# Kernel optimization log

Hardware: AMD Instinct MI355X
Metric: run time of the kernel (lower is better)

Reference implementation:

```python
import jax, jax.numpy as jnp
import numpy as np

B, T, D, H = 2, 4096, 512, 8
DH = D // H  # dim_head = 64


def setup_inputs() -> dict:
    key = jax.random.key(0)
    ks = jax.random.split(key, 10)
    s = 1.0 / np.sqrt(D)
    x = jax.random.normal(ks[0], (B, T, D), dtype=jnp.float32)
    Wq = jax.random.uniform(ks[1], (D, D), jnp.float32, -s, s)
    Wk = jax.random.uniform(ks[2], (D, D), jnp.float32, -s, s)
    Wv = jax.random.uniform(ks[3], (D, D), jnp.float32, -s, s)
    Wo = jax.random.uniform(ks[4], (D, D), jnp.float32, -s, s)
    bq = jnp.zeros((D,), jnp.float32)
    bk = jnp.zeros((D,), jnp.float32)
    bv = jnp.zeros((D,), jnp.float32)
    bo = jnp.zeros((D,), jnp.float32)
    mask = jax.random.randint(ks[5], (1, 1, T, T), 0, 2).astype(bool)
    return {"x": x, "Wq": Wq, "bq": bq, "Wk": Wk, "bk": bk,
            "Wv": Wv, "bv": bv, "Wo": Wo, "bo": bo, "mask": mask}


def reference(x, Wq, bq, Wk, bk, Wv, bv, Wo, bo, mask):
    # QKV projections (self-attention: Q=K=V=x)
    def split_heads(t):
        return t.reshape(B, T, H, DH).transpose(0, 2, 1, 3)  # (B,H,T,DH)
    Q = split_heads(x @ Wq + bq)
    K = split_heads(x @ Wk + bk)
    V = split_heads(x @ Wv + bv)
    # scaled dot-product attention with additive mask penalty (as in source)
    scores = jnp.einsum('bhqd,bhkd->bhqk', Q, K) / np.sqrt(DH)
    scores = scores + (~mask).astype(scores.dtype) * (-1e9)
    att_w = jax.nn.softmax(scores, axis=-1)
    O = jnp.einsum('bhqk,bhkd->bhqd', att_w, V)
    O = O.transpose(0, 2, 1, 3).reshape(B, T, D)
    return O @ Wo + bo
```

## Files before the change

### kernel.cpp

```cpp
#include <hip/hip_runtime.h>
#include <stdint.h>

#define B_ 2
#define T_ 4096
#define D_ 512
#define H_ 8
#define DH_ 64

typedef __bf16 bf16;
typedef __bf16 bf16x4_t __attribute__((ext_vector_type(4)));
typedef __bf16 bf16x8_t __attribute__((ext_vector_type(8)));
typedef float f32x4 __attribute__((ext_vector_type(4)));
typedef short short4_t __attribute__((ext_vector_type(4)));
typedef uint32_t u32;

static constexpr float QSCALE = 0.18033688011112042f;

__device__ __forceinline__ void async16(void* lds, const void* g) {
  __builtin_amdgcn_global_load_lds(
      (const __attribute__((address_space(1))) void*)g,
      (__attribute__((address_space(3))) void*)lds, 16, 0, 0);
}

__global__ __launch_bounds__(256) void prep_kernel(
    const float* __restrict__ x,
    const float* __restrict__ Wq, const float* __restrict__ Wk,
    const float* __restrict__ Wv, const float* __restrict__ Wo,
    const void* __restrict__ maskp,
    bf16* __restrict__ xb, bf16* __restrict__ WTall, bf16* __restrict__ WoT,
    u32* __restrict__ bmask)
{
  int bid = blockIdx.x;
  int tid = threadIdx.x;
  if (bid < 4096) {
    int idx = bid * 256 + tid;
    const float4* xf = (const float4*)x;
    float4 v = xf[idx];
    bf16x4_t o;
    o[0] = (bf16)v.x; o[1] = (bf16)v.y; o[2] = (bf16)v.z; o[3] = (bf16)v.w;
    ((bf16x4_t*)xb)[idx] = o;
  } else if (bid < 8192) {
    int gid = (bid - 4096) * 256 + tid;
    int sel = gid >> 18;
    int idx = gid & 262143;
    int n = idx >> 9, k = idx & 511;
    if (sel < 3) {
      const float* W = (sel == 0) ? Wq : (sel == 1) ? Wk : Wv;
      float v = W[k * 512 + n];
      if (sel == 0) v *= QSCALE;
      WTall[gid] = (bf16)v;
    } else {
      WoT[idx] = (bf16)Wo[k * 512 + n];
    }
  } else {
    int wid = (bid - 8192) * 256 + tid;
    const uint8_t* m8 = (const uint8_t*)maskp;
    bool u8mode = (__ballot(m8[4 * (tid & 63) + 1] != 0) != 0ull);
    int row = wid >> 7, wcol = wid & 127;
    size_t off = (size_t)row * 4096 + (size_t)wcol * 32;
    u32 w = 0;
    if (u8mode) {
      const uint4* p = (const uint4*)(m8 + off);
      uint4 a = p[0], b = p[1];
      u32 ws[8] = {a.x, a.y, a.z, a.w, b.x, b.y, b.z, b.w};
      #pragma unroll
      for (int j = 0; j < 32; ++j)
        if ((ws[j >> 2] >> ((j & 3) * 8)) & 0xffu) w |= (1u << j);
    } else {
      const uint4* p = (const uint4*)((const u32*)maskp + off);
      #pragma unroll
      for (int q = 0; q < 8; ++q) {
        uint4 a = p[q];
        if (a.x) w |= 1u << (q * 4 + 0);
        if (a.y) w |= 1u << (q * 4 + 1);
        if (a.z) w |= 1u << (q * 4 + 2);
        if (a.w) w |= 1u << (q * 4 + 3);
      }
    }
    bmask[((size_t)(row >> 6) * 64 + (wcol >> 1)) * 128 + (row & 63) * 2 + (wcol & 1)] = w;
  }
}

__global__ __launch_bounds__(256) void qkv_kernel(
    const bf16* __restrict__ xb, const bf16* __restrict__ WTall,
    const float* __restrict__ bq, const float* __restrict__ bk,
    const float* __restrict__ bv,
    bf16* __restrict__ Qb, bf16* __restrict__ Kb, bf16* __restrict__ Vtb)
{
  __shared__ char smem[32768];
  char* smX = smem;
  char* smW = smem + 16384;
  int tid = threadIdx.x;
  int lane = tid & 63, wave = tid >> 6;
  int lo = lane & 15, quad = lane >> 4;
  int wr = wave >> 1, wc = wave & 1;
  int bm = blockIdx.x * 128;
  int bn = blockIdx.y * 128;
  int sel = bn >> 9;
  f32x4 acc[4][4] = {};
  for (int kc = 0; kc < 8; ++kc) {
    __syncthreads();
    for (int s = tid; s < 1024; s += 256) {
      int row = s >> 3, slot = s & 7, cg = slot ^ (row & 7);
      async16(smX + s * 16, xb + (size_t)(bm + row) * 512 + kc * 64 + cg * 8);
      async16(smW + s * 16, WTall + (size_t)(bn + row) * 512 + kc * 64 + cg * 8);
    }
    __syncthreads();
    #pragma unroll
    for (int ks = 0; ks < 2; ++ks) {
      bf16x8_t a[4], b[4];
      #pragma unroll
      for (int mt = 0; mt < 4; ++mt) {
        int row = wr * 64 + mt * 16 + lo;
        int ch = (ks * 4 + quad) ^ (row & 7);
        a[mt] = *(const bf16x8_t*)(smX + row * 128 + ch * 16);
      }
      #pragma unroll
      for (int nt = 0; nt < 4; ++nt) {
        int row = wc * 64 + nt * 16 + lo;
        int ch = (ks * 4 + quad) ^ (row & 7);
        b[nt] = *(const bf16x8_t*)(smW + row * 128 + ch * 16);
      }
      if (sel == 2) {
        #pragma unroll
        for (int mt = 0; mt < 4; ++mt)
          #pragma unroll
          for (int nt = 0; nt < 4; ++nt)
            acc[mt][nt] = __builtin_amdgcn_mfma_f32_16x16x32_bf16(
                b[nt], a[mt], acc[mt][nt], 0, 0, 0);
      } else {
        #pragma unroll
        for (int mt = 0; mt < 4; ++mt)
          #pragma unroll
          for (int nt = 0; nt < 4; ++nt)
            acc[mt][nt] = __builtin_amdgcn_mfma_f32_16x16x32_bf16(
                a[mt], b[nt], acc[mt][nt], 0, 0, 0);
      }
    }
  }
  int b_ = bm >> 12;
  if (sel < 2) {
    #pragma unroll
    for (int mt = 0; mt < 4; ++mt) {
      #pragma unroll
      for (int nt = 0; nt < 4; ++nt) {
        int n0 = (bn + wc * 64 + nt * 16 + lo) & 511;
        int h = n0 >> 6, dh = n0 & 63;
        int m0 = bm + wr * 64 + mt * 16 + quad * 4;
        int t0 = m0 & 4095;
        float bias = (sel == 0) ? QSCALE * bq[n0] : bk[n0];
        bf16* dst = (sel == 0 ? Qb : Kb) + (size_t)(b_ * H_ + h) * T_ * DH_ + dh;
        #pragma unroll
        for (int r = 0; r < 4; ++r)
          dst[(size_t)(t0 + r) * 64] = (bf16)(acc[mt][nt][r] + bias);
      }
    }
  } else {
    #pragma unroll
    for (int mt = 0; mt < 4; ++mt) {
      #pragma unroll
      for (int nt = 0; nt < 4; ++nt) {
        int t0 = (bm & 4095) + wr * 64 + mt * 16 + lo;
        #pragma unroll
        for (int r = 0; r < 4; ++r) {
          int n0 = (bn & 511) + wc * 64 + nt * 16 + quad * 4 + r;
          float v = acc[mt][nt][r] + bv[n0];
          Vtb[((size_t)(b_ * H_ + (n0 >> 6)) * DH_ + (n0 & 63)) * T_ + t0] = (bf16)v;
        }
      }
    }
  }
}

__global__ __launch_bounds__(256, 4) void attn_kernel(
    const bf16* __restrict__ Qb, const bf16* __restrict__ Kb,
    const bf16* __restrict__ Vtb, const u32* __restrict__ bm2,
    bf16* __restrict__ Obuf)
{
  __shared__ char smem[16896];
  char* smK = smem;
  char* smV = smem + 8192;
  u32* smM = (u32*)(smem + 16384);
  int tid = threadIdx.x;
  int lane = tid & 63, wave = tid >> 6;
  int lo = lane & 15, quad = lane >> 4;
  int qh = wave & 1, kh = wave >> 1;
  int bh = blockIdx.x >> 6;
  int qt64 = blockIdx.x & 63;
  int qbase = qt64 * 64;

  const bf16* Qg = Qb + ((size_t)bh * T_ + qbase + qh * 32) * DH_;
  bf16x8_t qf[2][2];
  #pragma unroll
  for (int qt = 0; qt < 2; ++qt)
    #pragma unroll
    for (int ks = 0; ks < 2; ++ks)
      qf[qt][ks] = *(const bf16x8_t*)(Qg + (qt * 16 + lo) * 64 + ks * 32 + quad * 8);

  f32x4 O[2][4] = {};
  float lsum[2] = {0.f, 0.f};

  const bf16* Kg = Kb + (size_t)bh * T_ * DH_;
  const bf16* Vg = Vtb + (size_t)bh * DH_ * T_;
  const u32* mg = bm2 + (size_t)qt64 * 8192;

  for (int kc = 0; kc < 64; ++kc) {
    __syncthreads();
    for (int s = tid; s < 512; s += 256) {
      int row = s >> 3, slot = s & 7, cg = slot ^ (row & 7);
      async16(smK + s * 16, Kg + (size_t)(kc * 64 + row) * 64 + cg * 8);
      async16(smV + s * 16, Vg + (size_t)row * T_ + kc * 64 + cg * 8);
    }
    if (tid < 32) async16((char*)smM + tid * 16, mg + kc * 128 + tid * 4);
    __syncthreads();
    f32x4 St[2][2] = {};
    #pragma unroll
    for (int ks = 0; ks < 2; ++ks)
      #pragma unroll
      for (int kt = 0; kt < 2; ++kt) {
        int krow = kh * 32 + kt * 16 + lo;
        int ch = (ks * 4 + quad) ^ (krow & 7);
        bf16x8_t kf = *(const bf16x8_t*)(smK + krow * 128 + ch * 16);
        #pragma unroll
        for (int qt = 0; qt < 2; ++qt)
          St[kt][qt] = __builtin_amdgcn_mfma_f32_16x16x32_bf16(
              kf, qf[qt][ks], St[kt][qt], 0, 0, 0);
      }
    short4_t pf[2][2];
    #pragma unroll
    for (int qt = 0; qt < 2; ++qt) {
      u32 w = smM[(qh * 32 + qt * 16 + lo) * 2 + kh] >> (quad * 4);
      #pragma unroll
      for (int kt = 0; kt < 2; ++kt) {
        bf16x4_t t;
        #pragma unroll
        for (int r = 0; r < 4; ++r) {
          float p = ((w >> (kt * 16 + r)) & 1u)
                        ? __builtin_amdgcn_exp2f(St[kt][qt][r]) : 0.0f;
          lsum[qt] += p;
          t[r] = (bf16)p;
        }
        pf[qt][kt] = __builtin_bit_cast(short4_t, t);
      }
    }
    #pragma unroll
    for (int dt = 0; dt < 4; ++dt) {
      int d = dt * 16 + lo;
      #pragma unroll
      for (int kt = 0; kt < 2; ++kt) {
        int c0 = kh * 4 + kt * 2 + (quad >> 1);
        short4_t vf = *(const short4_t*)(
            smV + d * 128 + ((c0 ^ (d & 7)) << 4) + ((quad & 1) << 3));
        #pragma unroll
        for (int qt = 0; qt < 2; ++qt)
          O[qt][dt] = __builtin_amdgcn_mfma_f32_16x16x16bf16_1k(
              pf[qt][kt], vf, O[qt][dt], 0, 0, 0);
      }
    }
  }
  #pragma unroll
  for (int qt = 0; qt < 2; ++qt) {
    float v = lsum[qt];
    v += __shfl_xor(v, 16);
    v += __shfl_xor(v, 32);
    lsum[qt] = v;
  }
  __syncthreads();
  float* smO = (float*)smem;
  float* smL = (float*)(smem + 16384);
  if (kh == 1) {
    #pragma unroll
    for (int qt = 0; qt < 2; ++qt) {
      #pragma unroll
      for (int dt = 0; dt < 4; ++dt)
        #pragma unroll
        for (int r = 0; r < 4; ++r)
          smO[(qh * 32 + qt * 16 + quad * 4 + r) * 64 + dt * 16 + lo] = O[qt][dt][r];
      if (quad == 0) smL[qh * 32 + qt * 16 + lo] = lsum[qt];
    }
  }
  __syncthreads();
  if (kh == 0 && quad == 0) {
    #pragma unroll
    for (int qt = 0; qt < 2; ++qt)
      smL[qh * 32 + qt * 16 + lo] += lsum[qt];
  }
  __syncthreads();
  if (kh == 0) {
    bf16* Og = Obuf + ((size_t)bh * T_ + qbase + qh * 32) * DH_;
    #pragma unroll
    for (int qt = 0; qt < 2; ++qt) {
      #pragma unroll
      for (int r = 0; r < 4; ++r) {
        int rl = qt * 16 + quad * 4 + r;
        float inv = 1.0f / smL[qh * 32 + rl];
        #pragma unroll
        for (int dt = 0; dt < 4; ++dt) {
          float o = (O[qt][dt][r] + smO[(qh * 32 + rl) * 64 + dt * 16 + lo]) * inv;
          Og[(size_t)rl * 64 + dt * 16 + lo] = (bf16)o;
        }
      }
    }
  }
}

__global__ __launch_bounds__(256) void proj_kernel(
    const bf16* __restrict__ Obuf, const bf16* __restrict__ WoT,
    const float* __restrict__ bo, float* __restrict__ out)
{
  __shared__ char smem[32768];
  char* smA = smem;
  char* smW = smem + 16384;
  int tid = threadIdx.x;
  int lane = tid & 63, wave = tid >> 6;
  int lo = lane & 15, quad = lane >> 4;
  int wr = wave >> 1, wc = wave & 1;
  int bm = blockIdx.x * 128;
  int bn = blockIdx.y * 128;
  int b_ = bm >> 12, trow = bm & 4095;
  f32x4 acc[4][4] = {};
  for (int kc = 0; kc < 8; ++kc) {
    __syncthreads();
    const bf16* Ag = Obuf + ((size_t)(b_ * H_ + kc) * T_ + trow) * DH_;
    for (int s = tid; s < 1024; s += 256) {
      int row = s >> 3, slot = s & 7, cg = slot ^ (row & 7);
      async16(smA + s * 16, Ag + row * 64 + cg * 8);
      async16(smW + s * 16, WoT + (size_t)(bn + row) * 512 + kc * 64 + cg * 8);
    }
    __syncthreads();
    #pragma unroll
    for (int ks = 0; ks < 2; ++ks) {
      bf16x8_t a[4], b[4];
      #pragma unroll
      for (int mt = 0; mt < 4; ++mt) {
        int row = wr * 64 + mt * 16 + lo;
        int ch = (ks * 4 + quad) ^ (row & 7);
        a[mt] = *(const bf16x8_t*)(smA + row * 128 + ch * 16);
      }
      #pragma unroll
      for (int nt = 0; nt < 4; ++nt) {
        int row = wc * 64 + nt * 16 + lo;
        int ch = (ks * 4 + quad) ^ (row & 7);
        b[nt] = *(const bf16x8_t*)(smW + row * 128 + ch * 16);
      }
      #pragma unroll
      for (int mt = 0; mt < 4; ++mt)
        #pragma unroll
        for (int nt = 0; nt < 4; ++nt)
          acc[mt][nt] = __builtin_amdgcn_mfma_f32_16x16x32_bf16(
              a[mt], b[nt], acc[mt][nt], 0, 0, 0);
    }
  }
  #pragma unroll
  for (int mt = 0; mt < 4; ++mt) {
    #pragma unroll
    for (int nt = 0; nt < 4; ++nt) {
      int n_g = bn + wc * 64 + nt * 16 + lo;
      int m0 = bm + wr * 64 + mt * 16 + quad * 4;
      float bias = bo[n_g];
      #pragma unroll
      for (int r = 0; r < 4; ++r)
        out[(size_t)(m0 + r) * 512 + n_g] = acc[mt][nt][r] + bias;
    }
  }
}

extern "C" void kernel_launch(void* const* d_in, const int* in_sizes, int n_in,
                              void* d_out, int out_size, void* d_ws, size_t ws_size,
                              hipStream_t stream) {
  const float* x  = (const float*)d_in[0];
  const float* Wq = (const float*)d_in[1];
  const float* bq = (const float*)d_in[2];
  const float* Wk = (const float*)d_in[3];
  const float* bk = (const float*)d_in[4];
  const float* Wv = (const float*)d_in[5];
  const float* bv = (const float*)d_in[6];
  const float* Wo = (const float*)d_in[7];
  const float* bo = (const float*)d_in[8];
  const void* maskp = d_in[9];
  float* out = (float*)d_out;

  char* w = (char*)d_ws;
  bf16* xb    = (bf16*)(w);
  bf16* WTall = (bf16*)(w + 8388608);
  bf16* WoT   = (bf16*)(w + 9961472);
  bf16* Qb    = (bf16*)(w + 10485760);
  bf16* Kb    = (bf16*)(w + 18874368);
  bf16* Vtb   = (bf16*)(w + 27262976);
  bf16* Obuf  = (bf16*)(w + 35651584);
  u32*  bmask = (u32*)(w + 44040192);

  prep_kernel<<<10240, 256, 0, stream>>>(x, Wq, Wk, Wv, Wo, maskp,
                                         xb, WTall, WoT, bmask);
  qkv_kernel<<<dim3(64, 12), 256, 0, stream>>>(xb, WTall, bq, bk, bv,
                                               Qb, Kb, Vtb);
  attn_kernel<<<1024, 256, 0, stream>>>(Qb, Kb, Vtb, bmask, Obuf);
  proj_kernel<<<dim3(64, 4), 256, 0, stream>>>(Obuf, WoT, bo, out);
}
```

Measured before the change: 302.0 us.

## Vectorize GEMM epilogue stores via operand swap and compute softmax row sums with MFMA

In the QKV and output projection kernels, the MFMA operands are swapped so each lane holds four contiguous output columns (or, for V, four contiguous time steps). This lets the epilogues write 8-byte bf16x4 or 16-byte float4 vectors in place of strided scalar stores. In the attention kernel, the per-lane exp-sum accumulation and its cross-lane shuffles are replaced by an extra MFMA against a ones vector, and mask selection becomes a bitwise AND. This removes one sync from the reduction and adds some extra MFMA work per tile. A leftover dead assignment in the mask code is harmless.

```diff
diff --git a/kernel.cpp b/kernel.cpp
--- a/kernel.cpp
+++ b/kernel.cpp
@@ -121,7 +121,7 @@
         int ch = (ks * 4 + quad) ^ (row & 7);
         b[nt] = *(const bf16x8_t*)(smW + row * 128 + ch * 16);
       }
-      if (sel == 2) {
+      if (sel < 2) {
         #pragma unroll
         for (int mt = 0; mt < 4; ++mt)
           #pragma unroll
@@ -140,33 +140,39 @@
   }
   int b_ = bm >> 12;
   if (sel < 2) {
+    const float* bias = (sel == 0) ? bq : bk;
+    bf16* base = (sel == 0) ? Qb : Kb;
     #pragma unroll
     for (int mt = 0; mt < 4; ++mt) {
+      int t = (bm & 4095) + wr * 64 + mt * 16 + lo;
       #pragma unroll
       for (int nt = 0; nt < 4; ++nt) {
-        int n0 = (bn + wc * 64 + nt * 16 + lo) & 511;
-        int h = n0 >> 6, dh = n0 & 63;
-        int m0 = bm + wr * 64 + mt * 16 + quad * 4;
-        int t0 = m0 & 4095;
-        float bias = (sel == 0) ? QSCALE * bq[n0] : bk[n0];
-        bf16* dst = (sel == 0 ? Qb : Kb) + (size_t)(b_ * H_ + h) * T_ * DH_ + dh;
-        #pragma unroll
-        for (int r = 0; r < 4; ++r)
-          dst[(size_t)(t0 + r) * 64] = (bf16)(acc[mt][nt][r] + bias);
+        int n0 = (bn + wc * 64 + nt * 16 + quad * 4) & 511;
+        int h = n0 >> 6, dh0 = n0 & 63;
+        bf16x4_t v;
+        #pragma unroll
+        for (int r = 0; r < 4; ++r) {
+          float bs = bias[n0 + r];
+          if (sel == 0) bs *= QSCALE;
+          v[r] = (bf16)(acc[mt][nt][r] + bs);
+        }
+        *(bf16x4_t*)(base + (size_t)(b_ * H_ + h) * T_ * DH_ +
+                     (size_t)t * 64 + dh0) = v;
       }
     }
   } else {
     #pragma unroll
-    for (int mt = 0; mt < 4; ++mt) {
-      #pragma unroll
-      for (int nt = 0; nt < 4; ++nt) {
-        int t0 = (bm & 4095) + wr * 64 + mt * 16 + lo;
-        #pragma unroll
-        for (int r = 0; r < 4; ++r) {
-          int n0 = (bn & 511) + wc * 64 + nt * 16 + quad * 4 + r;
-          float v = acc[mt][nt][r] + bv[n0];
-          Vtb[((size_t)(b_ * H_ + (n0 >> 6)) * DH_ + (n0 & 63)) * T_ + t0] = (bf16)v;
-        }
+    for (int nt = 0; nt < 4; ++nt) {
+      int n0 = (bn + wc * 64 + nt * 16 + lo) & 511;
+      int h = n0 >> 6, dh = n0 & 63;
+      float bs = bv[n0];
+      #pragma unroll
+      for (int mt = 0; mt < 4; ++mt) {
+        int t0 = (bm & 4095) + wr * 64 + mt * 16 + quad * 4;
+        bf16x4_t v;
+        #pragma unroll
+        for (int r = 0; r < 4; ++r) v[r] = (bf16)(acc[mt][nt][r] + bs);
+        *(bf16x4_t*)(Vtb + ((size_t)(b_ * H_ + h) * DH_ + dh) * T_ + t0) = v;
       }
     }
   }
@@ -177,10 +183,12 @@
     const bf16* __restrict__ Vtb, const u32* __restrict__ bm2,
     bf16* __restrict__ Obuf)
 {
-  __shared__ char smem[16896];
+  __shared__ char smem[17408];
   char* smK = smem;
   char* smV = smem + 8192;
   u32* smM = (u32*)(smem + 16384);
+  float* smLa = (float*)(smem + 16896);
+  float* smLb = (float*)(smem + 17152);
   int tid = threadIdx.x;
   int lane = tid & 63, wave = tid >> 6;
   int lo = lane & 15, quad = lane >> 4;
@@ -197,8 +205,11 @@
     for (int ks = 0; ks < 2; ++ks)
       qf[qt][ks] = *(const bf16x8_t*)(Qg + (qt * 16 + lo) * 64 + ks * 32 + quad * 8);
 
+  short one = (lo == 0) ? (short)0x3F80 : (short)0;
+  short4_t ones = {one, one, one, one};
+
   f32x4 O[2][4] = {};
-  float lsum[2] = {0.f, 0.f};
+  f32x4 Ol[2] = {};
 
   const bf16* Kg = Kb + (size_t)bh * T_ * DH_;
   const bf16* Vg = Vtb + (size_t)bh * DH_ * T_;
@@ -235,14 +246,22 @@
         bf16x4_t t;
         #pragma unroll
         for (int r = 0; r < 4; ++r) {
-          float p = ((w >> (kt * 16 + r)) & 1u)
-                        ? __builtin_amdgcn_exp2f(St[kt][qt][r]) : 0.0f;
-          lsum[qt] += p;
-          t[r] = (bf16)p;
+          int mb = ((int)(w << (31 - (kt * 16 + r)))) >> 31;
+          u32 pe = __builtin_bit_cast(u32, __builtin_amdgcn_exp2f(St[kt][qt][r]));
+          t[r] = __builtin_bit_cast(bf16,
+                   (unsigned short)(__builtin_bit_cast(float, pe & (u32)mb) == 0.f
+                        ? 0 : 0));
+          t[r] = (bf16)__builtin_bit_cast(float, pe & (u32)mb);
         }
         pf[qt][kt] = __builtin_bit_cast(short4_t, t);
       }
     }
+    #pragma unroll
+    for (int kt = 0; kt < 2; ++kt)
+      #pragma unroll
+      for (int qt = 0; qt < 2; ++qt)
+        Ol[qt] = __builtin_amdgcn_mfma_f32_16x16x16bf16_1k(
+            pf[qt][kt], ones, Ol[qt], 0, 0, 0);
     #pragma unroll
     for (int dt = 0; dt < 4; ++dt) {
       int d = dt * 16 + lo;
@@ -258,32 +277,24 @@
       }
     }
   }
-  #pragma unroll
-  for (int qt = 0; qt < 2; ++qt) {
-    float v = lsum[qt];
-    v += __shfl_xor(v, 16);
-    v += __shfl_xor(v, 32);
-    lsum[qt] = v;
-  }
   __syncthreads();
   float* smO = (float*)smem;
-  float* smL = (float*)(smem + 16384);
+  if (lo == 0) {
+    float* dst = (kh == 0) ? smLa : smLb;
+    #pragma unroll
+    for (int qt = 0; qt < 2; ++qt)
+      #pragma unroll
+      for (int r = 0; r < 4; ++r)
+        dst[qh * 32 + qt * 16 + quad * 4 + r] = Ol[qt][r];
+  }
   if (kh == 1) {
     #pragma unroll
-    for (int qt = 0; qt < 2; ++qt) {
+    for (int qt = 0; qt < 2; ++qt)
       #pragma unroll
       for (int dt = 0; dt < 4; ++dt)
         #pragma unroll
         for (int r = 0; r < 4; ++r)
           smO[(qh * 32 + qt * 16 + quad * 4 + r) * 64 + dt * 16 + lo] = O[qt][dt][r];
-      if (quad == 0) smL[qh * 32 + qt * 16 + lo] = lsum[qt];
-    }
-  }
-  __syncthreads();
-  if (kh == 0 && quad == 0) {
-    #pragma unroll
-    for (int qt = 0; qt < 2; ++qt)
-      smL[qh * 32 + qt * 16 + lo] += lsum[qt];
   }
   __syncthreads();
   if (kh == 0) {
@@ -293,7 +304,7 @@
       #pragma unroll
       for (int r = 0; r < 4; ++r) {
         int rl = qt * 16 + quad * 4 + r;
-        float inv = 1.0f / smL[qh * 32 + rl];
+        float inv = 1.0f / (smLa[qh * 32 + rl] + smLb[qh * 32 + rl]);
         #pragma unroll
         for (int dt = 0; dt < 4; ++dt) {
           float o = (O[qt][dt][r] + smO[(qh * 32 + rl) * 64 + dt * 16 + lo]) * inv;
@@ -348,19 +359,21 @@
         #pragma unroll
         for (int nt = 0; nt < 4; ++nt)
           acc[mt][nt] = __builtin_amdgcn_mfma_f32_16x16x32_bf16(
-              a[mt], b[nt], acc[mt][nt], 0, 0, 0);
+              b[nt], a[mt], acc[mt][nt], 0, 0, 0);
     }
   }
   #pragma unroll
   for (int mt = 0; mt < 4; ++mt) {
+    int t = bm + wr * 64 + mt * 16 + lo;
     #pragma unroll
     for (int nt = 0; nt < 4; ++nt) {
-      int n_g = bn + wc * 64 + nt * 16 + lo;
-      int m0 = bm + wr * 64 + mt * 16 + quad * 4;
-      float bias = bo[n_g];
-      #pragma unroll
-      for (int r = 0; r < 4; ++r)
-        out[(size_t)(m0 + r) * 512 + n_g] = acc[mt][nt][r] + bias;
+      int c0 = bn + wc * 64 + nt * 16 + quad * 4;
+      float4 v;
+      v.x = acc[mt][nt][0] + bo[c0 + 0];
+      v.y = acc[mt][nt][1] + bo[c0 + 1];
+      v.z = acc[mt][nt][2] + bo[c0 + 2];
+      v.w = acc[mt][nt][3] + bo[c0 + 3];
+      *(float4*)(out + (size_t)t * 512 + c0) = v;
     }
   }
 }
```

Measured after the change: 296.0 us. 1.02x faster.
